# Performance work log

Hardware: AMD Instinct MI355X
Metric: run time of the kernel (lower is better)

Reference implementation:

```python
import jax, jax.numpy as jnp
import numpy as np

DIM = 128      # encoder output dim
D_OUT = 10     # num classes
T = 1.0        # temperature
EPS = 1e-7


def setup_inputs() -> dict:
    key = jax.random.key(0)
    ks = jax.random.split(key, 5)
    B, N, D_IN = 512, 100000, 128
    x = jax.random.normal(ks[0], (B, D_IN), jnp.float32)
    candidate_x = jax.random.normal(ks[1], (N, D_IN), jnp.float32)
    candidate_y = jax.random.randint(ks[2], (N,), 0, D_OUT, dtype=jnp.int32)
    W = jax.random.normal(ks[3], (DIM, D_IN), jnp.float32) / np.sqrt(D_IN).astype(np.float32)
    b = jax.random.normal(ks[4], (DIM,), jnp.float32) * 0.01
    return {"x": x, "candidate_x": candidate_x, "candidate_y": candidate_y, "W": W, "b": b}


def reference(x, candidate_x, candidate_y, W, b):
    # Linear encoder (n_blocks == 0 path)
    h = x @ W.T + b              # [B, DIM]
    hc = candidate_x @ W.T + b   # [N, DIM]
    # Pairwise L2 distances via the Gram expansion (same math as torch.cdist p=2)
    d2 = (jnp.sum(h * h, axis=-1, keepdims=True)
          + jnp.sum(hc * hc, axis=-1)[None, :]
          - 2.0 * (h @ hc.T))    # [B, N]
    dist = jnp.sqrt(jnp.maximum(d2, 0.0)) / T
    # Attention-like masked softmax over candidates (eval: no diagonal mask)
    p = jax.nn.softmax(-dist, axis=-1)              # [B, N]
    onehot_y = jax.nn.one_hot(candidate_y, D_OUT, dtype=p.dtype)  # [N, D_OUT]
    logits = p @ onehot_y                           # [B, D_OUT]
    return jnp.log(logits + EPS)
```

## Files before the change

### kernel.cpp

```cpp
#include <hip/hip_runtime.h>
#include <stdint.h>

typedef __bf16 bf16x8 __attribute__((ext_vector_type(8)));
typedef float f32x4 __attribute__((ext_vector_type(4)));
typedef short short8 __attribute__((ext_vector_type(8)));
typedef unsigned int uint2v __attribute__((ext_vector_type(2)));
typedef float float4_t __attribute__((ext_vector_type(4)));

union FragU { short8 s; bf16x8 b; };
union YbU { uint2v u2[2]; bf16x8 b; };

#define DEVI static __device__ __forceinline__

DEVI f32x4 mfma16(bf16x8 a, bf16x8 b, f32x4 c) {
  return __builtin_amdgcn_mfma_f32_16x16x32_bf16(a, b, c, 0, 0, 0);
}

DEVI bf16x8 cvt8(float4_t a, float4_t b) {
  bf16x8 r;
  r[0] = (__bf16)a[0]; r[1] = (__bf16)a[1]; r[2] = (__bf16)a[2]; r[3] = (__bf16)a[3];
  r[4] = (__bf16)b[0]; r[5] = (__bf16)b[1]; r[6] = (__bf16)b[2]; r[7] = (__bf16)b[3];
  return r;
}

__global__ __launch_bounds__(256) void setup_kernel(
    const float* __restrict__ W, unsigned short* __restrict__ Wbf,
    const int* __restrict__ y, unsigned short* __restrict__ YT,
    float* __restrict__ hcn, int N, int NP, int bpc) {
  const int bid = blockIdx.x, t = threadIdx.x;
  if (bid < 8) {
    int i = (bid * 256 + t) * 8;
    float4_t v0 = *(const float4_t*)(W + i);
    float4_t v1 = *(const float4_t*)(W + i + 4);
    FragU u; u.b = cvt8(v0, v1);
    *(short8*)(Wbf + i) = u.s;
  } else if (bid == 8) {
    int i = N + t;
    if (i < NP) hcn[i] = 1e30f;
  } else {
    int k = bid - 9;
    int c = k / bpc, j = k - c * bpc;
    int n0 = j * 2048 + t * 8;
    unsigned short* dst = YT + (size_t)c * NP + n0;
#pragma unroll
    for (int e = 0; e < 8; ++e) {
      int n = n0 + e;
      if (n < NP) dst[e] = (n < N && y[n] == c) ? 0x3F80u : 0u;
    }
  }
}

__global__ __launch_bounds__(256) void encode_kernel(
    const float* __restrict__ inA, const float* __restrict__ inB,
    const unsigned short* __restrict__ Wbf, const float* __restrict__ bias,
    unsigned short* __restrict__ outA, float* __restrict__ normA,
    unsigned short* __restrict__ outB, float* __restrict__ normB,
    int MA, int MB, int NBA) {
  const float* in;
  unsigned short* outh;
  float* outnorm;
  int M, blk;
  if ((int)blockIdx.x < NBA) {
    in = inA; outh = outA; outnorm = normA; M = MA; blk = blockIdx.x;
  } else {
    in = inB; outh = outB; outnorm = normB; M = MB; blk = blockIdx.x - NBA;
  }
  const int t = threadIdx.x, lane = t & 63, w = t >> 6;
  const int g = lane >> 4, q = lane & 15;
  const int rowbase = blk * 64 + w * 16;

  bf16x8 a[4];
  {
    int arow = rowbase + q;
    bool v = arow < M;
    int ar = v ? arow : 0;
#pragma unroll
    for (int kc = 0; kc < 4; ++kc) {
      const float4_t* p = (const float4_t*)(in + (size_t)ar * 128 + kc * 32 + g * 8);
      float4_t v0 = p[0], v1 = p[1];
      FragU u; u.b = cvt8(v0, v1);
      if (!v) u.s = short8{0, 0, 0, 0, 0, 0, 0, 0};
      a[kc] = u.b;
    }
  }

  f32x4 acc[8];
#pragma unroll
  for (int nt = 0; nt < 8; ++nt) acc[nt] = f32x4{0.f, 0.f, 0.f, 0.f};
#pragma unroll
  for (int nt = 0; nt < 8; ++nt) {
#pragma unroll
    for (int kc = 0; kc < 4; ++kc) {
      FragU u;
      u.s = *(const short8*)(Wbf + (size_t)(nt * 16 + q) * 128 + kc * 32 + g * 8);
      acc[nt] = mfma16(a[kc], u.b, acc[nt]);
    }
  }

  float nsq[4] = {0.f, 0.f, 0.f, 0.f};
#pragma unroll
  for (int nt = 0; nt < 8; ++nt) {
    int col = nt * 16 + q;
    float bv = bias[col];
#pragma unroll
    for (int r = 0; r < 4; ++r) {
      int row = rowbase + g * 4 + r;
      float val = acc[nt][r] + bv;
      __bf16 h = (__bf16)val;
      float vf = (float)h;
      nsq[r] += vf * vf;
      union { __bf16 h; unsigned short u; } cv; cv.h = h;
      if (row < M) outh[(size_t)row * 128 + col] = cv.u;
    }
  }
#pragma unroll
  for (int m = 1; m < 16; m <<= 1) {
#pragma unroll
    for (int r = 0; r < 4; ++r) nsq[r] += __shfl_xor(nsq[r], m, 64);
  }
  if (q == 0) {
#pragma unroll
    for (int r = 0; r < 4; ++r) {
      int row = rowbase + g * 4 + r;
      if (row < M) outnorm[row] = nsq[r];
    }
  }
}

__global__ __launch_bounds__(512, 4) void nca_main(
    const unsigned short* __restrict__ H, const float* __restrict__ hnorm,
    const unsigned short* __restrict__ HC, const float* __restrict__ hcnorm,
    const unsigned short* __restrict__ YT, float* __restrict__ part,
    int B, int BP, int N, int NP, int NT, int CHUNKS) {
  __shared__ __align__(16) unsigned short HCl[2][64 * 128];

  const int t = threadIdx.x, lane = t & 63, w = t >> 6;
  const int g = lane >> 4, q = lane & 15;
  const int rg = blockIdx.y, chunk = blockIdx.x;
  const int t0 = (int)(((long long)chunk * NT) / CHUNKS);
  const int t1 = (int)(((long long)(chunk + 1) * NT) / CHUNKS);

  bf16x8 hfrag[2][4];
  float hn[2];
  int hrow[2];
#pragma unroll
  for (int s = 0; s < 2; ++s) {
    hrow[s] = rg * 256 + s * 128 + w * 16 + q;
    bool v = hrow[s] < B;
    int ar = v ? hrow[s] : 0;
#pragma unroll
    for (int kc = 0; kc < 4; ++kc) {
      FragU u;
      u.s = *(const short8*)(H + (size_t)ar * 128 + kc * 32 + g * 8);
      if (!v) u.s = short8{0, 0, 0, 0, 0, 0, 0, 0};
      hfrag[s][kc] = u.b;
    }
    hn[s] = hnorm[ar];
  }

  f32x4 pool0 = f32x4{0.f, 0.f, 0.f, 0.f};
  f32x4 pool1 = f32x4{0.f, 0.f, 0.f, 0.f};

#define STAGE(TT, BUF)                                                        \
  {                                                                           \
    _Pragma("unroll") for (int i = 0; i < 2; ++i) {                           \
      int SI = t + 512 * i;                                                   \
      int row = SI >> 4, s = SI & 15;                                         \
      int srcslot = s ^ (row & 7);                                            \
      int cg = (TT)*64 + row;                                                 \
      if (cg >= N) cg = N - 1;                                                \
      const unsigned short* src = HC + (size_t)cg * 128 + srcslot * 8;        \
      char* ldsbase = (char*)HCl[BUF] + w * 1024 + i * 8192;                  \
      __builtin_amdgcn_global_load_lds(                                       \
          (const __attribute__((address_space(1))) unsigned int*)src,         \
          (__attribute__((address_space(3))) unsigned int*)ldsbase, 16, 0, 0);\
    }                                                                         \
  }

  int cur = 0;
  if (t0 < t1) STAGE(t0, 0);

  for (int tt = t0; tt < t1; ++tt) {
    __syncthreads();
    if (tt + 1 < t1) STAGE(tt + 1, cur ^ 1);

    const int colbase = tt * 64;
    float4_t cnv[4];
    uint2v ytu[4];
#pragma unroll
    for (int ns = 0; ns < 4; ++ns) {
      cnv[ns] = *(const float4_t*)(hcnorm + colbase + ns * 16 + g * 4);
      ytu[ns] = *(const uint2v*)(YT + (size_t)q * NP + colbase + ns * 16 + g * 4);
    }

#pragma unroll
    for (int ns = 0; ns < 4; ++ns) {
      int brow = ns * 16 + q;
      f32x4 a0 = f32x4{0.f, 0.f, 0.f, 0.f};
      f32x4 a1 = f32x4{0.f, 0.f, 0.f, 0.f};
#pragma unroll
      for (int kc = 0; kc < 4; ++kc) {
        int slot = (kc * 4 + g) ^ (brow & 7);
        FragU u;
        u.s = *(const short8*)((const char*)HCl[cur] + brow * 256 + slot * 16);
        a0 = mfma16(u.b, hfrag[0][kc], a0);
        a1 = mfma16(u.b, hfrag[1][kc], a1);
      }
      FragU wb0, wb1;
      wb0.s = short8{0, 0, 0, 0, 0, 0, 0, 0};
      wb1.s = short8{0, 0, 0, 0, 0, 0, 0, 0};
#pragma unroll
      for (int r = 0; r < 4; ++r) {
        float d20 = fmaf(-2.f, a0[r], hn[0] + cnv[ns][r]);
        float d21 = fmaf(-2.f, a1[r], hn[1] + cnv[ns][r]);
        d20 = fmaxf(d20, 0.f);
        d21 = fmaxf(d21, 0.f);
        float di0 = __builtin_amdgcn_sqrtf(d20);
        float di1 = __builtin_amdgcn_sqrtf(d21);
        wb0.b[r] = (__bf16)__expf(0.f - di0);
        wb1.b[r] = (__bf16)__expf(0.f - di1);
      }
      YbU yb;
      yb.u2[0] = ytu[ns];
      yb.u2[1] = uint2v{0u, 0u};
      pool0 = mfma16(yb.b, wb0.b, pool0);
      pool1 = mfma16(yb.b, wb1.b, pool1);
    }
    cur ^= 1;
  }
#undef STAGE

  if (hrow[0] < B)
    *(f32x4*)(part + ((size_t)chunk * BP + hrow[0]) * 16 + g * 4) = pool0;
  if (hrow[1] < B)
    *(f32x4*)(part + ((size_t)chunk * BP + hrow[1]) * 16 + g * 4) = pool1;
}

__global__ __launch_bounds__(64) void finalize_kernel(
    const float* __restrict__ part, float* __restrict__ out, int B, int BP,
    int CHUNKS) {
  const int row = blockIdx.x, t = threadIdx.x;
  const int c = t & 15, grp = t >> 4;
  float s = 0.f;
  for (int j = grp; j < CHUNKS; j += 4)
    s += part[((size_t)j * BP + row) * 16 + c];
  s += __shfl_xor(s, 16, 64);
  s += __shfl_xor(s, 32, 64);
  float Z = 0.f;
#pragma unroll
  for (int cc = 0; cc < 10; ++cc) Z += __shfl(s, cc, 64);
  if (t < 10) out[row * 10 + t] = logf(fmaf(s, 1.f / Z, 1e-7f));
}

extern "C" void kernel_launch(void* const* d_in, const int* in_sizes, int n_in,
                              void* d_out, int out_size, void* d_ws,
                              size_t ws_size, hipStream_t stream) {
  const float* x = (const float*)d_in[0];
  const float* cx = (const float*)d_in[1];
  const int* cy = (const int*)d_in[2];
  const float* W = (const float*)d_in[3];
  const float* b = (const float*)d_in[4];
  const int B = in_sizes[0] / 128;
  const int N = in_sizes[1] / 128;
  float* out = (float*)d_out;

  const int NT = (N + 63) / 64;
  const int NP = NT * 64;
  const int RG = (B + 255) / 256;
  const int BP = RG * 256;

  char* ws = (char*)d_ws;
  size_t o = 0;
  auto alloc = [&](size_t bytes) {
    size_t r = o;
    o += (bytes + 255) & ~(size_t)255;
    return r;
  };
  unsigned short* HC = (unsigned short*)(ws + alloc((size_t)N * 128 * 2));
  float* hcn = (float*)(ws + alloc((size_t)NP * 4));
  unsigned short* H = (unsigned short*)(ws + alloc((size_t)B * 128 * 2));
  float* hn = (float*)(ws + alloc((size_t)B * 4));
  unsigned short* Wbf = (unsigned short*)(ws + alloc(128 * 128 * 2));
  unsigned short* YT = (unsigned short*)(ws + alloc((size_t)16 * NP * 2));

  size_t avail = (ws_size > o) ? (ws_size - o) : 0;
  int CHUNKS = (int)(avail / ((size_t)BP * 16 * 4));
  if (CHUNKS > 256) CHUNKS = 256;
  if (CHUNKS < 32) CHUNKS = 32;
  float* part = (float*)(ws + alloc((size_t)CHUNKS * BP * 16 * 4));

  const int bpc = (NP + 2047) / 2048;
  setup_kernel<<<9 + 16 * bpc, 256, 0, stream>>>(W, Wbf, cy, YT, hcn, N, NP, bpc);

  const int NBA = (N + 63) / 64, NBB = (B + 63) / 64;
  encode_kernel<<<NBA + NBB, 256, 0, stream>>>(cx, x, Wbf, b, HC, hcn, H, hn,
                                               N, B, NBA);

  dim3 grid(CHUNKS, RG);
  nca_main<<<grid, 512, 0, stream>>>(H, hn, HC, hcn, YT, part, B, BP, N, NP,
                                     NT, CHUNKS);
  finalize_kernel<<<B, 64, 0, stream>>>(part, out, B, BP, CHUNKS);
}
```

Measured before the change: 176.7 us.

## Fuse setup into encode kernel, stage W in LDS, transpose partials layout

Merges the setup and encode launches into one kernel. Each encode block converts W to bf16 itself and keeps it in swizzled shared memory, so the separate Wbf buffer and its global reads go away. The main kernel's occupancy hint rises from 4 to 6 and the chunk cap from 256 to 384. Partial sums are stored row-major per batch row so the finalize reduction reads contiguous memory, with 4 rows per block. The risks are that every encode block now re-reads and re-converts all of W, and that the higher occupancy hint may force register spills.

```diff
diff --git a/kernel.cpp b/kernel.cpp
--- a/kernel.cpp
+++ b/kernel.cpp
@@ -23,65 +23,84 @@
   return r;
 }
 
-__global__ __launch_bounds__(256) void setup_kernel(
-    const float* __restrict__ W, unsigned short* __restrict__ Wbf,
-    const int* __restrict__ y, unsigned short* __restrict__ YT,
-    float* __restrict__ hcn, int N, int NP, int bpc) {
+__global__ __launch_bounds__(256) void prep_encode_kernel(
+    const float* __restrict__ cx, const float* __restrict__ x,
+    const float* __restrict__ W, const float* __restrict__ bias,
+    const int* __restrict__ y,
+    unsigned short* __restrict__ HC, float* __restrict__ hcn,
+    unsigned short* __restrict__ Hm, float* __restrict__ hnm,
+    unsigned short* __restrict__ YT,
+    int N, int Bm, int NP, int NBA, int NBB, int bpc) {
+  __shared__ __align__(16) unsigned short Wl[128 * 128];
+
   const int bid = blockIdx.x, t = threadIdx.x;
-  if (bid < 8) {
-    int i = (bid * 256 + t) * 8;
-    float4_t v0 = *(const float4_t*)(W + i);
-    float4_t v1 = *(const float4_t*)(W + i + 4);
-    FragU u; u.b = cvt8(v0, v1);
-    *(short8*)(Wbf + i) = u.s;
-  } else if (bid == 8) {
-    int i = N + t;
-    if (i < NP) hcn[i] = 1e30f;
-  } else {
-    int k = bid - 9;
-    int c = k / bpc, j = k - c * bpc;
-    int n0 = j * 2048 + t * 8;
-    unsigned short* dst = YT + (size_t)c * NP + n0;
-#pragma unroll
-    for (int e = 0; e < 8; ++e) {
-      int n = n0 + e;
-      if (n < NP) dst[e] = (n < N && y[n] == c) ? 0x3F80u : 0u;
-    }
-  }
-}
-
-__global__ __launch_bounds__(256) void encode_kernel(
-    const float* __restrict__ inA, const float* __restrict__ inB,
-    const unsigned short* __restrict__ Wbf, const float* __restrict__ bias,
-    unsigned short* __restrict__ outA, float* __restrict__ normA,
-    unsigned short* __restrict__ outB, float* __restrict__ normB,
-    int MA, int MB, int NBA) {
+  const int NB_ENC = NBA + NBB;
+
+  if (bid >= NB_ENC) {
+    if (bid == NB_ENC) {
+      int i = N + t;
+      if (i < NP) hcn[i] = 1e30f;
+    } else {
+      int k = bid - NB_ENC - 1;
+      int c = k / bpc, j = k - c * bpc;
+      int n0 = j * 2048 + t * 8;
+      unsigned short* dst = YT + (size_t)c * NP + n0;
+#pragma unroll
+      for (int e = 0; e < 8; ++e) {
+        int n = n0 + e;
+        if (n < NP) dst[e] = (n < N && y[n] == c) ? 0x3F80u : 0u;
+      }
+    }
+    return;
+  }
+
   const float* in;
   unsigned short* outh;
   float* outnorm;
   int M, blk;
-  if ((int)blockIdx.x < NBA) {
-    in = inA; outh = outA; outnorm = normA; M = MA; blk = blockIdx.x;
+  if (bid < NBA) {
+    in = cx; outh = HC; outnorm = hcn; M = N; blk = bid;
   } else {
-    in = inB; outh = outB; outnorm = normB; M = MB; blk = blockIdx.x - NBA;
-  }
-  const int t = threadIdx.x, lane = t & 63, w = t >> 6;
+    in = x; outh = Hm; outnorm = hnm; M = Bm; blk = bid - NBA;
+  }
+
+  const int lane = t & 63, w = t >> 6;
   const int g = lane >> 4, q = lane & 15;
   const int rowbase = blk * 64 + w * 16;
 
-  bf16x8 a[4];
+  float4_t iv[8];
+  const int arow = rowbase + q;
+  const bool av = arow < M;
   {
-    int arow = rowbase + q;
-    bool v = arow < M;
-    int ar = v ? arow : 0;
+    int ar = av ? arow : 0;
 #pragma unroll
     for (int kc = 0; kc < 4; ++kc) {
       const float4_t* p = (const float4_t*)(in + (size_t)ar * 128 + kc * 32 + g * 8);
-      float4_t v0 = p[0], v1 = p[1];
+      iv[2 * kc] = p[0];
+      iv[2 * kc + 1] = p[1];
+    }
+  }
+
+  {
+    int row = t >> 1, half = t & 1;
+    const float* wsrc = W + row * 128 + half * 64;
+#pragma unroll
+    for (int j = 0; j < 8; ++j) {
+      float4_t v0 = *(const float4_t*)(wsrc + j * 8);
+      float4_t v1 = *(const float4_t*)(wsrc + j * 8 + 4);
       FragU u; u.b = cvt8(v0, v1);
-      if (!v) u.s = short8{0, 0, 0, 0, 0, 0, 0, 0};
-      a[kc] = u.b;
-    }
+      int slot = (half * 8 + j) ^ (row & 7);
+      *(short8*)((char*)Wl + row * 256 + slot * 16) = u.s;
+    }
+  }
+  __syncthreads();
+
+  bf16x8 a[4];
+#pragma unroll
+  for (int kc = 0; kc < 4; ++kc) {
+    FragU u; u.b = cvt8(iv[2 * kc], iv[2 * kc + 1]);
+    if (!av) u.s = short8{0, 0, 0, 0, 0, 0, 0, 0};
+    a[kc] = u.b;
   }
 
   f32x4 acc[8];
@@ -89,10 +108,12 @@
   for (int nt = 0; nt < 8; ++nt) acc[nt] = f32x4{0.f, 0.f, 0.f, 0.f};
 #pragma unroll
   for (int nt = 0; nt < 8; ++nt) {
+    int brow = nt * 16 + q;
 #pragma unroll
     for (int kc = 0; kc < 4; ++kc) {
+      int slot = (kc * 4 + g) ^ (brow & 7);
       FragU u;
-      u.s = *(const short8*)(Wbf + (size_t)(nt * 16 + q) * 128 + kc * 32 + g * 8);
+      u.s = *(const short8*)((const char*)Wl + brow * 256 + slot * 16);
       acc[nt] = mfma16(a[kc], u.b, acc[nt]);
     }
   }
@@ -127,11 +148,11 @@
   }
 }
 
-__global__ __launch_bounds__(512, 4) void nca_main(
+__global__ __launch_bounds__(512, 6) void nca_main(
     const unsigned short* __restrict__ H, const float* __restrict__ hnorm,
     const unsigned short* __restrict__ HC, const float* __restrict__ hcnorm,
     const unsigned short* __restrict__ YT, float* __restrict__ part,
-    int B, int BP, int N, int NP, int NT, int CHUNKS) {
+    int B, int N, int NP, int NT, int CHUNKS) {
   __shared__ __align__(16) unsigned short HCl[2][64 * 128];
 
   const int t = threadIdx.x, lane = t & 63, w = t >> 6;
@@ -231,19 +252,21 @@
 #undef STAGE
 
   if (hrow[0] < B)
-    *(f32x4*)(part + ((size_t)chunk * BP + hrow[0]) * 16 + g * 4) = pool0;
+    *(f32x4*)(part + ((size_t)hrow[0] * CHUNKS + chunk) * 16 + g * 4) = pool0;
   if (hrow[1] < B)
-    *(f32x4*)(part + ((size_t)chunk * BP + hrow[1]) * 16 + g * 4) = pool1;
-}
-
-__global__ __launch_bounds__(64) void finalize_kernel(
-    const float* __restrict__ part, float* __restrict__ out, int B, int BP,
+    *(f32x4*)(part + ((size_t)hrow[1] * CHUNKS + chunk) * 16 + g * 4) = pool1;
+}
+
+__global__ __launch_bounds__(256) void finalize_kernel(
+    const float* __restrict__ part, float* __restrict__ out, int B,
     int CHUNKS) {
-  const int row = blockIdx.x, t = threadIdx.x;
+  const int w = threadIdx.x >> 6, t = threadIdx.x & 63;
+  const int row = blockIdx.x * 4 + w;
+  if (row >= B) return;
   const int c = t & 15, grp = t >> 4;
+  const float* p = part + (size_t)row * CHUNKS * 16;
   float s = 0.f;
-  for (int j = grp; j < CHUNKS; j += 4)
-    s += part[((size_t)j * BP + row) * 16 + c];
+  for (int j = grp; j < CHUNKS; j += 4) s += p[j * 16 + c];
   s += __shfl_xor(s, 16, 64);
   s += __shfl_xor(s, 32, 64);
   float Z = 0.f;
@@ -267,7 +290,6 @@
   const int NT = (N + 63) / 64;
   const int NP = NT * 64;
   const int RG = (B + 255) / 256;
-  const int BP = RG * 256;
 
   char* ws = (char*)d_ws;
   size_t o = 0;
@@ -280,24 +302,21 @@
   float* hcn = (float*)(ws + alloc((size_t)NP * 4));
   unsigned short* H = (unsigned short*)(ws + alloc((size_t)B * 128 * 2));
   float* hn = (float*)(ws + alloc((size_t)B * 4));
-  unsigned short* Wbf = (unsigned short*)(ws + alloc(128 * 128 * 2));
   unsigned short* YT = (unsigned short*)(ws + alloc((size_t)16 * NP * 2));
 
   size_t avail = (ws_size > o) ? (ws_size - o) : 0;
-  int CHUNKS = (int)(avail / ((size_t)BP * 16 * 4));
-  if (CHUNKS > 256) CHUNKS = 256;
+  int CHUNKS = (int)(avail / ((size_t)B * 16 * 4));
+  if (CHUNKS > 384) CHUNKS = 384;
   if (CHUNKS < 32) CHUNKS = 32;
-  float* part = (float*)(ws + alloc((size_t)CHUNKS * BP * 16 * 4));
-
+  float* part = (float*)(ws + alloc((size_t)CHUNKS * B * 16 * 4));
+
+  const int NBA = (N + 63) / 64, NBB = (B + 63) / 64;
   const int bpc = (NP + 2047) / 2048;
-  setup_kernel<<<9 + 16 * bpc, 256, 0, stream>>>(W, Wbf, cy, YT, hcn, N, NP, bpc);
-
-  const int NBA = (N + 63) / 64, NBB = (B + 63) / 64;
-  encode_kernel<<<NBA + NBB, 256, 0, stream>>>(cx, x, Wbf, b, HC, hcn, H, hn,
-                                               N, B, NBA);
+  prep_encode_kernel<<<NBA + NBB + 1 + 16 * bpc, 256, 0, stream>>>(
+      cx, x, W, b, cy, HC, hcn, H, hn, YT, N, B, NP, NBA, NBB, bpc);
 
   dim3 grid(CHUNKS, RG);
-  nca_main<<<grid, 512, 0, stream>>>(H, hn, HC, hcn, YT, part, B, BP, N, NP,
-                                     NT, CHUNKS);
-  finalize_kernel<<<B, 64, 0, stream>>>(part, out, B, BP, CHUNKS);
-}
+  nca_main<<<grid, 512, 0, stream>>>(H, hn, HC, hcn, YT, part, B, N, NP, NT,
+                                     CHUNKS);
+  finalize_kernel<<<(B + 3) / 4, 256, 0, stream>>>(part, out, B, CHUNKS);
+}
```

Result: slower. 184.7 us (+4.5%).
